# Optimization experiments

Measured on AMD Instinct MI355X. Metric: run time of the kernel, lower is better.

## Reference

```python
import jax, jax.numpy as jnp
import numpy as np

D = 1024

def setup_inputs() -> dict:
    key = jax.random.key(0)
    ks = jax.random.split(key, 7)
    s = 1.0 / np.sqrt(D)
    x = jax.random.normal(ks[0], (4, 4096, D), dtype=jnp.float32)
    Wi = jax.random.uniform(ks[1], (2 * D, D), jnp.float32, -s, s)   # in_proj weight [2D, D]
    bi = jax.random.uniform(ks[2], (2 * D,), jnp.float32, -s, s)
    Wc = jax.random.uniform(ks[3], (D, 1, 3), jnp.float32, -0.577, 0.577)  # depthwise conv [D,1,3]
    bc = jax.random.uniform(ks[4], (D,), jnp.float32, -0.577, 0.577)
    Wo = jax.random.uniform(ks[5], (D, D), jnp.float32, -s, s)       # out_proj weight [D, D]
    bo = jax.random.uniform(ks[6], (D,), jnp.float32, -s, s)
    return {"x": x, "Wi": Wi, "bi": bi, "Wc": Wc, "bc": bc, "Wo": Wo, "bo": bo}

def _depthwise_conv1d(v, Wc, bc):
    # v: [B, L, D] -> NCH [B, D, L]; kernel [D, 1, 3] (OIH), groups = D; pad 1 both sides
    y = jax.lax.conv_general_dilated(
        v.transpose(0, 2, 1), Wc,
        window_strides=(1,), padding=[(1, 1)],
        dimension_numbers=("NCH", "OIH", "NCH"),
        feature_group_count=v.shape[-1])
    return y.transpose(0, 2, 1) + bc  # [B, L, D]

def reference(x, Wi, bi, Wc, bc, Wo, bo):
    uv = jnp.einsum("bld,ed->ble", x, Wi) + bi        # [B, L, 2D]
    u, v = jnp.split(uv, 2, axis=-1)                   # each [B, L, D]
    y = _depthwise_conv1d(v, Wc, bc)
    y = jax.nn.silu(y) * u                             # fused gate
    return jnp.einsum("bld,ed->ble", y, Wo) + bo       # [B, L, D]
```

## Files before the change

kernel.cpp:

```cpp
#include <hip/hip_runtime.h>
#include <math.h>


typedef __attribute__((ext_vector_type(8))) short short8;
typedef __attribute__((ext_vector_type(4))) float floatx4;

__device__ __forceinline__ float b2f(short s) {
    unsigned int u = ((unsigned int)(unsigned short)s) << 16;
    float f;
    __builtin_memcpy(&f, &u, 4);
    return f;
}

__device__ __forceinline__ short f2b(float f) {
    unsigned int u;
    __builtin_memcpy(&u, &f, 4);
    u += 0x7fffu + ((u >> 16) & 1u);
    return (short)(u >> 16);
}

__device__ __forceinline__ void gl_lds16(const short* g, short* l) {
    __builtin_amdgcn_global_load_lds(
        (const __attribute__((address_space(1))) unsigned int*)g,
        (__attribute__((address_space(3))) unsigned int*)l,
        16, 0, 0);
}

__global__ __launch_bounds__(256) void cvt_all(
    const float* __restrict__ x, const float* __restrict__ Wi,
    const float* __restrict__ Wo, short* __restrict__ xb,
    short* __restrict__ Wib, short* __restrict__ Wob)
{
    constexpr int n1 = 16384 * 1024 / 8;
    constexpr int n2 = 2048 * 1024 / 8;
    constexpr int n3 = 1024 * 1024 / 8;
    int i = blockIdx.x * 256 + threadIdx.x;
    const float* src;
    short* dst;
    int j;
    if (i < n1)           { src = x;  dst = xb;  j = i; }
    else if (i < n1 + n2) { src = Wi; dst = Wib; j = i - n1; }
    else if (i < n1 + n2 + n3) { src = Wo; dst = Wob; j = i - n1 - n2; }
    else return;
    float4 a = ((const float4*)src)[2 * j];
    float4 b = ((const float4*)src)[2 * j + 1];
    short8 o;
    o[0] = f2b(a.x); o[1] = f2b(a.y); o[2] = f2b(a.z); o[3] = f2b(a.w);
    o[4] = f2b(b.x); o[5] = f2b(b.y); o[6] = f2b(b.z); o[7] = f2b(b.w);
    ((short8*)dst)[j] = o;
}

template <bool OUTF32>
__global__ __launch_bounds__(512, 2) void gemm_bt(
    const short* __restrict__ A, const short* __restrict__ B,
    const float* __restrict__ bias, void* __restrict__ Cv,
    int lda, int ldb, int ldc)
{
    constexpr int K  = 1024;
    constexpr int NT = K / 32;
    __shared__ __attribute__((aligned(16))) short As[4 * 8192];
    __shared__ __attribute__((aligned(16))) short Bs[4 * 8192];

    const int tid  = threadIdx.x;
    const int wave = tid >> 6;
    const int lane = tid & 63;
    const int mBase = blockIdx.y * 256;
    const int nBase = blockIdx.x * 256;

    floatx4 acc[8][4];
#pragma unroll
    for (int i = 0; i < 8; i++)
#pragma unroll
        for (int j = 0; j < 4; j++) acc[i][j] = {0.f, 0.f, 0.f, 0.f};

    const int srow = lane >> 2;
    const int sg   = ((lane & 3) ^ ((srow >> 1) & 3)) * 8;
    const short* gA = A + (size_t)(mBase + wave * 32 + srow) * lda + sg;
    const short* gB = B + (size_t)(nBase + wave * 32 + srow) * ldb + sg;
    short* lA0 = &As[wave * 1024];
    short* lB0 = &Bs[wave * 1024];

    auto stage = [&](int kk, int slot) {
#pragma unroll
        for (int j = 0; j < 2; j++) {
            gl_lds16(gA + (size_t)(16 * j) * lda + kk, lA0 + slot * 8192 + j * 512);
            gl_lds16(gB + (size_t)(16 * j) * ldb + kk, lB0 + slot * 8192 + j * 512);
        }
    };

    const int fRow = lane & 15;
    const int lg   = lane >> 4;
    const int pg8  = (lg ^ ((fRow >> 1) & 3)) * 8;
    const int mq   = (wave >> 2) * 128;
    const int nq   = (wave & 3) * 64;
    const int aBase = (mq + fRow) * 32 + pg8;
    const int bBase = (nq + fRow) * 32 + pg8;

    auto compute = [&](int slot) {
        const short* Ab = &As[slot * 8192];
        const short* Bb = &Bs[slot * 8192];
        short8 av[8], bv[4];
#pragma unroll
        for (int mi = 0; mi < 8; mi++)
            av[mi] = *(const short8*)&Ab[aBase + mi * 512];
#pragma unroll
        for (int ni = 0; ni < 4; ni++)
            bv[ni] = *(const short8*)&Bb[bBase + ni * 512];
        __builtin_amdgcn_s_setprio(1);
#pragma unroll
        for (int mi = 0; mi < 8; mi++)
#pragma unroll
            for (int ni = 0; ni < 4; ni++)
                acc[mi][ni] = __builtin_amdgcn_mfma_f32_16x16x32_bf16(
                    av[mi], bv[ni], acc[mi][ni], 0, 0, 0);
        __builtin_amdgcn_s_setprio(0);
    };

    stage(0, 0);
    stage(32, 1);
    stage(64, 2);

    for (int t = 0; t < NT - 3; ++t) {
        stage((t + 3) * 32, (t + 3) & 3);
        asm volatile("s_waitcnt vmcnt(12)" ::: "memory");
        __builtin_amdgcn_s_barrier();
        asm volatile("" ::: "memory");
        compute(t & 3);
        asm volatile("" ::: "memory");
        __builtin_amdgcn_s_barrier();
        asm volatile("" ::: "memory");
    }

    asm volatile("s_waitcnt vmcnt(8)" ::: "memory");
    __builtin_amdgcn_s_barrier();
    asm volatile("" ::: "memory");
    compute((NT - 3) & 3);
    __builtin_amdgcn_s_barrier();
    asm volatile("s_waitcnt vmcnt(4)" ::: "memory");
    __builtin_amdgcn_s_barrier();
    asm volatile("" ::: "memory");
    compute((NT - 2) & 3);
    __builtin_amdgcn_s_barrier();
    asm volatile("s_waitcnt vmcnt(0)" ::: "memory");
    __builtin_amdgcn_s_barrier();
    asm volatile("" ::: "memory");
    compute((NT - 1) & 3);

    const int colq = lane & 15;
    const int rowq = lg * 4;
#pragma unroll
    for (int ni = 0; ni < 4; ni++) {
        const int col = nBase + nq + ni * 16 + colq;
        const float bvv = bias[col];
#pragma unroll
        for (int mi = 0; mi < 8; mi++) {
            const int row = mBase + mq + mi * 16 + rowq;
#pragma unroll
            for (int r = 0; r < 4; r++) {
                float v = acc[mi][ni][r] + bvv;
                if (OUTF32)
                    ((float*)Cv)[(size_t)(row + r) * ldc + col] = v;
                else
                    ((short*)Cv)[(size_t)(row + r) * ldc + col] = f2b(v);
            }
        }
    }
}

__global__ __launch_bounds__(256) void conv_gate(
    const short* __restrict__ uv, const float* __restrict__ Wc,
    const float* __restrict__ bc, short* __restrict__ yb)
{
    const int idx = blockIdx.x * 256 + threadIdx.x;
    const int d8 = idx & 127;
    const int m  = idx >> 7;
    const int l  = m & 4095;
    const int d  = d8 * 8;

    float w[24];
#pragma unroll
    for (int q = 0; q < 6; q++)
        *(float4*)&w[q * 4] = ((const float4*)(Wc + d * 3))[q];
    float bcv[8];
    *(float4*)&bcv[0] = ((const float4*)(bc + d))[0];
    *(float4*)&bcv[4] = ((const float4*)(bc + d))[1];

    const size_t rowu = (size_t)m * 2048 + d;
    const size_t rowv = rowu + 1024;

    const short8 z = {0, 0, 0, 0, 0, 0, 0, 0};
    const short8 us = *(const short8*)(uv + rowu);
    const short8 vc = *(const short8*)(uv + rowv);
    const short8 vm = (l > 0)    ? *(const short8*)(uv + rowv - 2048) : z;
    const short8 vp = (l < 4095) ? *(const short8*)(uv + rowv + 2048) : z;

    short8 outv;
#pragma unroll
    for (int j = 0; j < 8; j++) {
        float y = b2f(vm[j]) * w[j * 3 + 0]
                + b2f(vc[j]) * w[j * 3 + 1]
                + b2f(vp[j]) * w[j * 3 + 2]
                + bcv[j];
        float sil = y / (1.0f + expf(-y));
        outv[j] = f2b(sil * b2f(us[j]));
    }
    *(short8*)(yb + (size_t)m * 1024 + d) = outv;
}

extern "C" void kernel_launch(void* const* d_in, const int* in_sizes, int n_in,
                              void* d_out, int out_size, void* d_ws, size_t ws_size,
                              hipStream_t stream)
{
    const float* x  = (const float*)d_in[0];
    const float* Wi = (const float*)d_in[1];
    const float* bi = (const float*)d_in[2];
    const float* Wc = (const float*)d_in[3];
    const float* bc = (const float*)d_in[4];
    const float* Wo = (const float*)d_in[5];
    const float* bo = (const float*)d_in[6];
    float* out = (float*)d_out;

    short* wsS = (short*)d_ws;
    short* uv  = wsS;
    short* xb  = uv + (size_t)16384 * 2048;
    short* Wib = xb + (size_t)16384 * 1024;
    short* Wob = Wib + (size_t)2048 * 1024;

    dim3 blk(256);
    dim3 blkG(512);

    constexpr int nCvt = (16384 * 1024 + 2048 * 1024 + 1024 * 1024) / 8;
    cvt_all<<<(nCvt + 255) / 256, blk, 0, stream>>>(x, Wi, Wo, xb, Wib, Wob);

    dim3 g1(2048 / 256, 16384 / 256);
    gemm_bt<false><<<g1, blkG, 0, stream>>>(xb, Wib, bi, uv, 1024, 1024, 2048);

    conv_gate<<<(16384 * 128) / 256, blk, 0, stream>>>(uv, Wc, bc, xb);

    dim3 g2(1024 / 256, 16384 / 256);
    gemm_bt<true><<<g2, blkG, 0, stream>>>(xb, Wob, bo, out, 1024, 1024, 1024);
}
```

Measured before the change: 310.9 us.

## Split GEMM K-tile into two MFMA phases with interleaved staging and XCD remap

After: 288.2 us. 7.3% less time.

```diff
diff --git a/kernel.cpp b/kernel.cpp
--- a/kernel.cpp
+++ b/kernel.cpp
@@ -50,22 +50,68 @@
     ((short8*)dst)[j] = o;
 }
 
+#define GB_TILE(SLOT, WAIT, ST)                                              \
+  {                                                                          \
+    asm volatile(WAIT ::: "memory");                                         \
+    __builtin_amdgcn_s_barrier();                                            \
+    asm volatile("" ::: "memory");                                           \
+    if ((ST) >= 0) {                                                         \
+        gl_lds16(gA + (size_t)(ST) * 32, lA0 + ((ST) & 3) * 8192);           \
+        gl_lds16(gA + (size_t)(ST) * 32 + (size_t)16 * lda,                  \
+                 lA0 + ((ST) & 3) * 8192 + 512);                             \
+    }                                                                        \
+    const short* Ab = &As[(SLOT) * 8192];                                    \
+    const short* Bb = &Bs[(SLOT) * 8192];                                    \
+    short8 av0[4], av1[4], bvv[4];                                           \
+    _Pragma("unroll") for (int ni = 0; ni < 4; ni++)                         \
+        bvv[ni] = *(const short8*)&Bb[bBase + ni * 512];                     \
+    _Pragma("unroll") for (int mi = 0; mi < 4; mi++)                         \
+        av0[mi] = *(const short8*)&Ab[aBase + mi * 512];                     \
+    asm volatile("s_waitcnt lgkmcnt(0)" ::: "memory");                       \
+    __builtin_amdgcn_sched_barrier(0);                                       \
+    __builtin_amdgcn_s_setprio(1);                                           \
+    _Pragma("unroll") for (int mi = 0; mi < 4; mi++)                         \
+      _Pragma("unroll") for (int ni = 0; ni < 4; ni++)                       \
+        acc[mi][ni] = __builtin_amdgcn_mfma_f32_16x16x32_bf16(               \
+            av0[mi], bvv[ni], acc[mi][ni], 0, 0, 0);                         \
+    __builtin_amdgcn_s_setprio(0);                                           \
+    __builtin_amdgcn_s_barrier();                                            \
+    asm volatile("" ::: "memory");                                           \
+    if ((ST) >= 0) {                                                         \
+        gl_lds16(gB + (size_t)(ST) * 32, lB0 + ((ST) & 3) * 8192);           \
+        gl_lds16(gB + (size_t)(ST) * 32 + (size_t)16 * ldb,                  \
+                 lB0 + ((ST) & 3) * 8192 + 512);                             \
+    }                                                                        \
+    _Pragma("unroll") for (int mi = 0; mi < 4; mi++)                         \
+        av1[mi] = *(const short8*)&Ab[aBase + (4 + mi) * 512];               \
+    asm volatile("s_waitcnt lgkmcnt(0)" ::: "memory");                       \
+    __builtin_amdgcn_sched_barrier(0);                                       \
+    __builtin_amdgcn_s_setprio(1);                                           \
+    _Pragma("unroll") for (int mi = 0; mi < 4; mi++)                         \
+      _Pragma("unroll") for (int ni = 0; ni < 4; ni++)                       \
+        acc[4 + mi][ni] = __builtin_amdgcn_mfma_f32_16x16x32_bf16(           \
+            av1[mi], bvv[ni], acc[4 + mi][ni], 0, 0, 0);                     \
+    __builtin_amdgcn_s_setprio(0);                                           \
+  }
+
 template <bool OUTF32>
 __global__ __launch_bounds__(512, 2) void gemm_bt(
     const short* __restrict__ A, const short* __restrict__ B,
     const float* __restrict__ bias, void* __restrict__ Cv,
     int lda, int ldb, int ldc)
 {
-    constexpr int K  = 1024;
-    constexpr int NT = K / 32;
     __shared__ __attribute__((aligned(16))) short As[4 * 8192];
     __shared__ __attribute__((aligned(16))) short Bs[4 * 8192];
 
     const int tid  = threadIdx.x;
     const int wave = tid >> 6;
     const int lane = tid & 63;
-    const int mBase = blockIdx.y * 256;
-    const int nBase = blockIdx.x * 256;
+
+    const int nwg = gridDim.x * gridDim.y;
+    const int f   = blockIdx.y * gridDim.x + blockIdx.x;
+    const int nf  = (f & 7) * (nwg >> 3) + (f >> 3);
+    const int mBase = (nf / gridDim.x) * 256;
+    const int nBase = (nf % gridDim.x) * 256;
 
     floatx4 acc[8][4];
 #pragma unroll
@@ -79,14 +125,6 @@
     const short* gB = B + (size_t)(nBase + wave * 32 + srow) * ldb + sg;
     short* lA0 = &As[wave * 1024];
     short* lB0 = &Bs[wave * 1024];
-
-    auto stage = [&](int kk, int slot) {
-#pragma unroll
-        for (int j = 0; j < 2; j++) {
-            gl_lds16(gA + (size_t)(16 * j) * lda + kk, lA0 + slot * 8192 + j * 512);
-            gl_lds16(gB + (size_t)(16 * j) * ldb + kk, lB0 + slot * 8192 + j * 512);
-        }
-    };
 
     const int fRow = lane & 15;
     const int lg   = lane >> 4;
@@ -96,68 +134,37 @@
     const int aBase = (mq + fRow) * 32 + pg8;
     const int bBase = (nq + fRow) * 32 + pg8;
 
-    auto compute = [&](int slot) {
-        const short* Ab = &As[slot * 8192];
-        const short* Bb = &Bs[slot * 8192];
-        short8 av[8], bv[4];
-#pragma unroll
-        for (int mi = 0; mi < 8; mi++)
-            av[mi] = *(const short8*)&Ab[aBase + mi * 512];
-#pragma unroll
-        for (int ni = 0; ni < 4; ni++)
-            bv[ni] = *(const short8*)&Bb[bBase + ni * 512];
-        __builtin_amdgcn_s_setprio(1);
-#pragma unroll
-        for (int mi = 0; mi < 8; mi++)
-#pragma unroll
-            for (int ni = 0; ni < 4; ni++)
-                acc[mi][ni] = __builtin_amdgcn_mfma_f32_16x16x32_bf16(
-                    av[mi], bv[ni], acc[mi][ni], 0, 0, 0);
-        __builtin_amdgcn_s_setprio(0);
-    };
-
-    stage(0, 0);
-    stage(32, 1);
-    stage(64, 2);
-
-    for (int t = 0; t < NT - 3; ++t) {
-        stage((t + 3) * 32, (t + 3) & 3);
-        asm volatile("s_waitcnt vmcnt(12)" ::: "memory");
-        __builtin_amdgcn_s_barrier();
-        asm volatile("" ::: "memory");
-        compute(t & 3);
-        asm volatile("" ::: "memory");
-        __builtin_amdgcn_s_barrier();
-        asm volatile("" ::: "memory");
-    }
-
-    asm volatile("s_waitcnt vmcnt(8)" ::: "memory");
-    __builtin_amdgcn_s_barrier();
-    asm volatile("" ::: "memory");
-    compute((NT - 3) & 3);
-    __builtin_amdgcn_s_barrier();
-    asm volatile("s_waitcnt vmcnt(4)" ::: "memory");
-    __builtin_amdgcn_s_barrier();
-    asm volatile("" ::: "memory");
-    compute((NT - 2) & 3);
-    __builtin_amdgcn_s_barrier();
-    asm volatile("s_waitcnt vmcnt(0)" ::: "memory");
-    __builtin_amdgcn_s_barrier();
-    asm volatile("" ::: "memory");
-    compute((NT - 1) & 3);
+#pragma unroll
+    for (int p = 0; p < 3; p++) {
+        gl_lds16(gA + (size_t)p * 32, lA0 + p * 8192);
+        gl_lds16(gA + (size_t)p * 32 + (size_t)16 * lda, lA0 + p * 8192 + 512);
+        gl_lds16(gB + (size_t)p * 32, lB0 + p * 8192);
+        gl_lds16(gB + (size_t)p * 32 + (size_t)16 * ldb, lB0 + p * 8192 + 512);
+    }
+
+    for (int tb = 0; tb < 28; tb += 4) {
+        GB_TILE(0, "s_waitcnt vmcnt(8)", tb + 3)
+        GB_TILE(1, "s_waitcnt vmcnt(8)", tb + 4)
+        GB_TILE(2, "s_waitcnt vmcnt(8)", tb + 5)
+        GB_TILE(3, "s_waitcnt vmcnt(8)", tb + 6)
+    }
+    GB_TILE(0, "s_waitcnt vmcnt(8)", 31)
+    GB_TILE(1, "s_waitcnt vmcnt(8)", -1)
+    GB_TILE(2, "s_waitcnt vmcnt(4)", -1)
+    GB_TILE(3, "s_waitcnt vmcnt(0)", -1)
 
     const int colq = lane & 15;
     const int rowq = lg * 4;
 #pragma unroll
     for (int ni = 0; ni < 4; ni++) {
         const int col = nBase + nq + ni * 16 + colq;
-        const float bvv = bias[col];
+        const float bvv2 = bias[col];
 #pragma unroll
         for (int mi = 0; mi < 8; mi++) {
             const int row = mBase + mq + mi * 16 + rowq;
 #pragma unroll
             for (int r = 0; r < 4; r++) {
-                float v = acc[mi][ni][r] + bvv;
+                float v = acc[mi][ni][r] + bvv2;
                 if (OUTF32)
                     ((float*)Cv)[(size_t)(row + r) * ldc + col] = v;
                 else
```
